# Kernel tuning notes

Hardware: AMD Instinct MI355X
Metric: run time of the kernel (lower is better)

## Reference

```python
import jax, jax.numpy as jnp
import numpy as np

D_MODEL = 1024
N_HEADS = 16
D_K = D_MODEL // N_HEADS

def _xavier(key, shape):
    fan_in, fan_out = shape[1], shape[0]
    limit = float(np.sqrt(6.0 / (fan_in + fan_out)))
    return jax.random.uniform(key, shape, jnp.float32, -limit, limit)

def setup_inputs() -> dict:
    key = jax.random.key(0)
    ks = jax.random.split(key, 7)
    B, S = 2, 2048
    return {
        "query": jax.random.normal(ks[0], (B, S, D_MODEL), jnp.float32),
        "key": jax.random.normal(ks[1], (B, S, D_MODEL), jnp.float32),
        "value": jax.random.normal(ks[2], (B, S, D_MODEL), jnp.float32),
        "w_q": _xavier(ks[3], (D_MODEL, D_MODEL)),  # torch Linear weight [out, in]
        "w_k": _xavier(ks[4], (D_MODEL, D_MODEL)),
        "w_v": _xavier(ks[5], (D_MODEL, D_MODEL)),
        "w_o": _xavier(ks[6], (D_MODEL, D_MODEL)),
        "ln_gamma": jnp.ones((D_MODEL,), jnp.float32),
        "ln_beta": jnp.zeros((D_MODEL,), jnp.float32),
    }

def reference(query, key, value, w_q, w_k, w_v, w_o, ln_gamma, ln_beta):
    B, S, _ = query.shape
    # projections (torch Linear: x @ W.T), split into heads -> [B, H, S, d_k]
    def split_heads(x, W):
        return (x @ W.T).reshape(B, S, N_HEADS, D_K).transpose(0, 2, 1, 3)
    Q = split_heads(query, w_q)
    K = split_heads(key, w_k)
    V = split_heads(value, w_v)
    scores = jnp.einsum('bhqd,bhkd->bhqk', Q, K) / jnp.sqrt(jnp.float32(D_K))
    attn = jax.nn.softmax(scores, axis=-1)  # dropout disabled (p=0 / eval)
    ctx = jnp.einsum('bhqk,bhkd->bhqd', attn, V)
    ctx = ctx.transpose(0, 2, 1, 3).reshape(B, S, D_MODEL)
    out = ctx @ w_o.T
    # residual + LayerNorm
    x = query + out
    mu = jnp.mean(x, axis=-1, keepdims=True)
    var = jnp.var(x, axis=-1, keepdims=True)
    return (x - mu) / jnp.sqrt(var + 1e-5) * ln_gamma + ln_beta
```

## Files before the change

### kernel.cpp

```cpp
#include <hip/hip_runtime.h>
#include <hip/hip_bf16.h>

#define DEVI __device__ __forceinline__

typedef float f32x4 __attribute__((ext_vector_type(4)));
typedef short bf16x8 __attribute__((ext_vector_type(8)));
typedef unsigned short ushort_t;

DEVI ushort_t f2bf(float x) {
  union { float f; unsigned u; } c; c.f = x;
  unsigned u = c.u;
  unsigned r = (u + 0x7fffu + ((u >> 16) & 1u)) >> 16;
  return (ushort_t)r;
}

DEVI float bf2f(unsigned hw) {
  union { unsigned u; float f; } c; c.u = hw << 16; return c.f;
}

DEVI unsigned cvt_pk_bf16(float lo, float hi) {
  unsigned r;
  asm volatile("v_cvt_pk_bf16_f32 %0, %1, %2" : "=v"(r) : "v"(lo), "v"(hi));
  return r;
}

DEVI void gload16(const ushort_t* g, ushort_t* l) {
  __builtin_amdgcn_global_load_lds(
      (const __attribute__((address_space(1))) unsigned int*)g,
      (__attribute__((address_space(3))) unsigned int*)l, 16, 0, 0);
}

#define WAITL0() asm volatile("s_waitcnt lgkmcnt(0)" ::: "memory")


__global__ __launch_bounds__(256)
void cvt_all_kernel(const float* __restrict__ p0, const float* __restrict__ p1,
                    const float* __restrict__ p2,
                    const float* __restrict__ w0, const float* __restrict__ w1,
                    const float* __restrict__ w2, const float* __restrict__ w3,
                    ushort_t* __restrict__ o0, ushort_t* __restrict__ o1,
                    ushort_t* __restrict__ o2,
                    ushort_t* __restrict__ q0, ushort_t* __restrict__ q1,
                    ushort_t* __restrict__ q2, ushort_t* __restrict__ q3) {
  int z = blockIdx.y;
  int i = blockIdx.x * 256 + threadIdx.x;
  const float* in;
  ushort_t* out;
  if (z < 3) {
    in = (z == 0) ? p0 : (z == 1) ? p1 : p2;
    out = (z == 0) ? o0 : (z == 1) ? o1 : o2;
  } else {
    int w = i >> 17;
    int local = i & 131071;
    in = ((w == 0) ? w0 : (w == 1) ? w1 : (w == 2) ? w2 : w3);
    out = ((w == 0) ? q0 : (w == 1) ? q1 : (w == 2) ? q2 : q3);
    i = local;
  }
  const float4* p = (const float4*)in + (size_t)i * 2;
  float4 a = p[0], b = p[1];
  uint4 v;
  v.x = cvt_pk_bf16(a.x, a.y);
  v.y = cvt_pk_bf16(a.z, a.w);
  v.z = cvt_pk_bf16(b.x, b.y);
  v.w = cvt_pk_bf16(b.z, b.w);
  ((uint4*)out)[i] = v;
}


__global__ __launch_bounds__(256)
void gemm128(const ushort_t* __restrict__ A0, const ushort_t* __restrict__ A1,
             const ushort_t* __restrict__ A2,
             const ushort_t* __restrict__ W0, const ushort_t* __restrict__ W1,
             const ushort_t* __restrict__ W2,
             void* __restrict__ O0, void* __restrict__ O1,
             void* __restrict__ O2, int mode_base, int nsteps, float qscale) {
  constexpr int K = 1024;
  int z = blockIdx.z;
  int mode = (mode_base == 3) ? 3 : mode_base + z;
  const ushort_t* A = (z == 0) ? A0 : (z == 1) ? A1 : A2;
  const ushort_t* W = (z == 0) ? W0 : (z == 1) ? W1 : W2;
  void* Op = (z == 0) ? O0 : (z == 1) ? O1 : O2;
  if (mode == 3) {
    A = A0 + z * 512;
    W = W0 + z * 512;
    Op = z ? O1 : O0;
  }
  float scale = (mode == 0) ? qscale : 1.0f;
  int m0 = (mode == 2) ? blockIdx.y * 128 : blockIdx.x * 128;
  int n0 = (mode == 2) ? blockIdx.x * 128 : blockIdx.y * 128;

  __shared__ __align__(16) ushort_t Asm[128 * 64];
  __shared__ __align__(16) ushort_t Bsm[128 * 64];

  int t = threadIdx.x;
  int lane = t & 63, wave = t >> 6;
  int wm = wave >> 1, wn = wave & 1;
  int col = lane & 15, g = lane >> 4;
  int lr = lane >> 3, lc = lane & 7;
  int cswz = col & 7;

  const ushort_t* aSrc = A + (size_t)(m0 + wave * 32 + lr) * K + (lc ^ lr) * 8;
  const ushort_t* bSrc = W + (size_t)(n0 + wave * 32 + lr) * K + (lc ^ lr) * 8;

  f32x4 z4 = {0.f, 0.f, 0.f, 0.f};
  f32x4 acc[4][4];
  for (int i = 0; i < 4; i++)
    for (int j = 0; j < 4; j++) acc[i][j] = z4;

  for (int kt = 0; kt < nsteps; ++kt) {
    int koff = kt * 64;
#pragma unroll
    for (int i_ = 0; i_ < 4; i_++) {
      gload16(aSrc + koff + i_ * 8 * K, &Asm[(wave * 32 + i_ * 8) * 64]);
      gload16(bSrc + koff + i_ * 8 * K, &Bsm[(wave * 32 + i_ * 8) * 64]);
    }
    __syncthreads();
#pragma unroll
    for (int kk = 0; kk < 2; ++kk) {
      bf16x8 af[4], bfr[4];
#pragma unroll
      for (int mi = 0; mi < 4; mi++) {
        int row = wm * 64 + mi * 16 + col;
        af[mi] = *(const bf16x8*)(Asm + row * 64 + (((kk * 4 + g) ^ cswz) * 8));
      }
#pragma unroll
      for (int ni = 0; ni < 4; ni++) {
        int row = wn * 64 + ni * 16 + col;
        bfr[ni] = *(const bf16x8*)(Bsm + row * 64 + (((kk * 4 + g) ^ cswz) * 8));
      }
      __builtin_amdgcn_s_setprio(1);
#pragma unroll
      for (int mi = 0; mi < 4; mi++)
#pragma unroll
        for (int ni = 0; ni < 4; ni++)
          acc[mi][ni] = __builtin_amdgcn_mfma_f32_16x16x32_bf16(af[mi], bfr[ni],
                                                                acc[mi][ni], 0, 0, 0);
      __builtin_amdgcn_s_setprio(0);
    }
    __syncthreads();
  }

#pragma unroll
  for (int mi = 0; mi < 4; mi++)
#pragma unroll
    for (int ni = 0; ni < 4; ni++)
#pragma unroll
      for (int r = 0; r < 4; r++) {
        int m = m0 + wm * 64 + mi * 16 + g * 4 + r;
        int n = n0 + wn * 64 + ni * 16 + col;
        float v = acc[mi][ni][r] * scale;
        if (mode <= 1) {
          int b = m >> 11, s = m & 2047, h = n >> 6, d = n & 63;
          ((ushort_t*)Op)[(((size_t)(b * 16 + h) * 2048 + s) * 64) + d] = f2bf(v);
        } else if (mode == 2) {
          int h = m >> 6, d = m & 63, b = n >> 11, s = n & 2047;
          ((ushort_t*)Op)[(((size_t)(b * 16 + h) * 64 + d) * 2048) + s] = f2bf(v);
        } else {
          ((ushort_t*)Op)[(size_t)m * 1024 + n] = f2bf(v);
        }
      }
}


__global__ __launch_bounds__(256, 4)
void attn_kernel(const ushort_t* __restrict__ Qh, const ushort_t* __restrict__ Kh,
                 const ushort_t* __restrict__ Vt,
                 ushort_t* __restrict__ op0, ushort_t* __restrict__ op1,
                 float* __restrict__ lp0, float* __restrict__ lp1) {
  int qt = blockIdx.x;
  int bh = blockIdx.y;
  int sp = blockIdx.z;
  int t = threadIdx.x, lane = t & 63, wave = t >> 6;
  int col = lane & 15, g = lane >> 4;
  int lr = lane >> 3, lc = lane & 7;
  int cswz = col & 7;
  int q0 = qt * 128 + wave * 32;
  int kbase = sp * 1024;
  ushort_t* opart = sp ? op1 : op0;
  float* lpart = sp ? lp1 : lp0;

  const ushort_t* Qp = Qh + (size_t)bh * 2048 * 64;
  const ushort_t* Kp = Kh + (size_t)bh * 2048 * 64;
  const ushort_t* Vp = Vt + (size_t)bh * 64 * 2048;

  __shared__ __align__(16) ushort_t Ksm[2][64 * 64];
  __shared__ __align__(16) ushort_t Vsm[2][64 * 64];

  int slot0 = wave * 16 + lr;
  int slot1 = slot0 + 8;
  int key0 = (slot0 & 0x20) | ((slot0 & 0x0C) << 1) | ((slot0 & 0x10) >> 2) | (slot0 & 3);
  int key1 = (slot1 & 0x20) | ((slot1 & 0x0C) << 1) | ((slot1 & 0x10) >> 2) | (slot1 & 3);

  const ushort_t* kSrc0 = Kp + (size_t)key0 * 64 + (lc ^ lr) * 8;
  const ushort_t* kSrc1 = Kp + (size_t)key1 * 64 + (lc ^ lr) * 8;
  const ushort_t* vSrc = Vp + (size_t)(wave * 16 + lr) * 2048 + (lc ^ lr) * 8;

#define ATTN_STAGE(buf, k0) do { \
    gload16(kSrc0 + (size_t)(k0) * 64, &Ksm[buf][wave * 1024]);        \
    gload16(kSrc1 + (size_t)(k0) * 64, &Ksm[buf][wave * 1024 + 512]);  \
    gload16(vSrc + (k0),               &Vsm[buf][wave * 1024]);        \
    gload16(vSrc + (k0) + 16384,       &Vsm[buf][wave * 1024 + 512]);  \
  } while (0)

  bf16x8 qa0 = *(const bf16x8*)(Qp + (size_t)(q0 + col) * 64 + g * 8);
  bf16x8 qa1 = *(const bf16x8*)(Qp + (size_t)(q0 + col) * 64 + 32 + g * 8);
  bf16x8 qb0 = *(const bf16x8*)(Qp + (size_t)(q0 + 16 + col) * 64 + g * 8);
  bf16x8 qb1 = *(const bf16x8*)(Qp + (size_t)(q0 + 16 + col) * 64 + 32 + g * 8);

  f32x4 z4 = {0.f, 0.f, 0.f, 0.f};
  f32x4 oa[4], ob[4];
  for (int i = 0; i < 4; i++) { oa[i] = z4; ob[i] = z4; }
  f32x4 la = z4, lb = z4;

  ATTN_STAGE(0, kbase);
  __syncthreads();

  for (int it = 0; it < 16; ++it) {
    int cur = it & 1;
    int k0 = kbase + it * 64;
    if (it < 15) ATTN_STAGE(cur ^ 1, k0 + 64);

    const ushort_t* Ks = Ksm[cur];
    const ushort_t* Vs = Vsm[cur];

    f32x4 sa[4], sb[4];
#pragma unroll
    for (int kt = 0; kt < 4; kt++) {
      int off = (kt * 16 + col) * 64 + ((g ^ cswz) * 8);
      bf16x8 kf0 = *(const bf16x8*)(Ks + off);
      bf16x8 kf1 = *(const bf16x8*)(Ks + (off ^ 32));
      f32x4 a = z4, b = z4;
      __builtin_amdgcn_s_setprio(1);
      a = __builtin_amdgcn_mfma_f32_16x16x32_bf16(kf0, qa0, a, 0, 0, 0);
      a = __builtin_amdgcn_mfma_f32_16x16x32_bf16(kf1, qa1, a, 0, 0, 0);
      b = __builtin_amdgcn_mfma_f32_16x16x32_bf16(kf0, qb0, b, 0, 0, 0);
      b = __builtin_amdgcn_mfma_f32_16x16x32_bf16(kf1, qb1, b, 0, 0, 0);
      __builtin_amdgcn_s_setprio(0);
      sa[kt] = a; sb[kt] = b;
    }

    unsigned pka[8], pkb[8];
#pragma unroll
    for (int kt = 0; kt < 4; kt++) {
      float a0 = __builtin_amdgcn_exp2f(sa[kt][0]);
      float a1 = __builtin_amdgcn_exp2f(sa[kt][1]);
      float a2 = __builtin_amdgcn_exp2f(sa[kt][2]);
      float a3 = __builtin_amdgcn_exp2f(sa[kt][3]);
      la[0] += a0; la[1] += a1; la[2] += a2; la[3] += a3;
      pka[2 * kt]     = cvt_pk_bf16(a0, a1);
      pka[2 * kt + 1] = cvt_pk_bf16(a2, a3);
      float b0 = __builtin_amdgcn_exp2f(sb[kt][0]);
      float b1 = __builtin_amdgcn_exp2f(sb[kt][1]);
      float b2 = __builtin_amdgcn_exp2f(sb[kt][2]);
      float b3 = __builtin_amdgcn_exp2f(sb[kt][3]);
      lb[0] += b0; lb[1] += b1; lb[2] += b2; lb[3] += b3;
      pkb[2 * kt]     = cvt_pk_bf16(b0, b1);
      pkb[2 * kt + 1] = cvt_pk_bf16(b2, b3);
    }

#pragma unroll
    for (int kk = 0; kk < 2; kk++) {
      union { uint4 u; bf16x8 f; } ua, ub;
      ua.u.x = pka[4 * kk];     ua.u.y = pka[4 * kk + 1];
      ua.u.z = pka[4 * kk + 2]; ua.u.w = pka[4 * kk + 3];
      ub.u.x = pkb[4 * kk];     ub.u.y = pkb[4 * kk + 1];
      ub.u.z = pkb[4 * kk + 2]; ub.u.w = pkb[4 * kk + 3];
      __builtin_amdgcn_s_setprio(1);
#pragma unroll
      for (int dt = 0; dt < 4; dt++) {
        bf16x8 vf = *(const bf16x8*)(Vs + (dt * 16 + col) * 64 +
                                     (((kk * 4 + g) ^ cswz) * 8));
        oa[dt] = __builtin_amdgcn_mfma_f32_16x16x32_bf16(vf, ua.f, oa[dt], 0, 0, 0);
        ob[dt] = __builtin_amdgcn_mfma_f32_16x16x32_bf16(vf, ub.f, ob[dt], 0, 0, 0);
      }
      __builtin_amdgcn_s_setprio(0);
    }
    __syncthreads();
  }
#undef ATTN_STAGE

  float lva = (la[0] + la[1]) + (la[2] + la[3]);
  lva += __shfl_xor(lva, 16);
  lva += __shfl_xor(lva, 32);
  float lvb = (lb[0] + lb[1]) + (lb[2] + lb[3]);
  lvb += __shfl_xor(lvb, 16);
  lvb += __shfl_xor(lvb, 32);
  if (g == 0) {
    lpart[(size_t)bh * 2048 + q0 + col] = lva;
    lpart[(size_t)bh * 2048 + q0 + 16 + col] = lvb;
  }
  int b = bh >> 4, h = bh & 15;
#pragma unroll
  for (int dt = 0; dt < 4; dt++)
#pragma unroll
    for (int r = 0; r < 4; r++) {
      int d = dt * 16 + g * 4 + r;
      opart[((size_t)(b * 2048 + q0 + col)) * 1024 + h * 64 + d] =
          f2bf(oa[dt][r]);
      opart[((size_t)(b * 2048 + q0 + 16 + col)) * 1024 + h * 64 + d] =
          f2bf(ob[dt][r]);
    }
}


__global__ __launch_bounds__(256)
void attn_reduce(const ushort_t* __restrict__ o0, const ushort_t* __restrict__ o1,
                 const float* __restrict__ l0, const float* __restrict__ l1,
                 ushort_t* __restrict__ ctx) {
  int m = blockIdx.x;
  int t = threadIdx.x;
  int b = m >> 11, q = m & 2047;
  int h = t >> 4;
  size_t li = (size_t)(b * 16 + h) * 2048 + q;
  float inv = 1.0f / (l0[li] + l1[li]);
  uint2 a = ((const uint2*)(o0 + (size_t)m * 1024))[t];
  uint2 c = ((const uint2*)(o1 + (size_t)m * 1024))[t];
  float x0 = (bf2f(a.x & 0xffffu) + bf2f(c.x & 0xffffu)) * inv;
  float x1 = (bf2f(a.x >> 16)     + bf2f(c.x >> 16))     * inv;
  float x2 = (bf2f(a.y & 0xffffu) + bf2f(c.y & 0xffffu)) * inv;
  float x3 = (bf2f(a.y >> 16)     + bf2f(c.y >> 16))     * inv;
  uint2 o;
  o.x = cvt_pk_bf16(x0, x1);
  o.y = cvt_pk_bf16(x2, x3);
  ((uint2*)(ctx + (size_t)m * 1024))[t] = o;
}


__global__ __launch_bounds__(256)
void ln_kernel(const float* __restrict__ resid, const ushort_t* __restrict__ p0,
               const ushort_t* __restrict__ p1,
               const float* __restrict__ gamma, const float* __restrict__ beta,
               float* __restrict__ out) {
  int m = blockIdx.x;
  int t = threadIdx.x;
  int lane = t & 63, wave = t >> 6;
  float4 a = ((const float4*)(resid + (size_t)m * 1024))[t];
  uint2 v0 = ((const uint2*)(p0 + (size_t)m * 1024))[t];
  uint2 v1 = ((const uint2*)(p1 + (size_t)m * 1024))[t];
  float4 x;
  x.x = a.x + bf2f(v0.x & 0xffffu) + bf2f(v1.x & 0xffffu);
  x.y = a.y + bf2f(v0.x >> 16)     + bf2f(v1.x >> 16);
  x.z = a.z + bf2f(v0.y & 0xffffu) + bf2f(v1.y & 0xffffu);
  x.w = a.w + bf2f(v0.y >> 16)     + bf2f(v1.y >> 16);
  float sum = (x.x + x.y) + (x.z + x.w);
  float ssq = x.x * x.x + x.y * x.y + x.z * x.z + x.w * x.w;
  for (int off = 1; off < 64; off <<= 1) {
    sum += __shfl_xor(sum, off);
    ssq += __shfl_xor(ssq, off);
  }
  __shared__ float red[8];
  if (lane == 0) { red[wave] = sum; red[4 + wave] = ssq; }
  __syncthreads();
  sum = red[0] + red[1] + red[2] + red[3];
  ssq = red[4] + red[5] + red[6] + red[7];
  float mu = sum * (1.f / 1024.f);
  float var = ssq * (1.f / 1024.f) - mu * mu;
  float rstd = rsqrtf(var + 1e-5f);
  const float4* gp = (const float4*)gamma;
  const float4* bp = (const float4*)beta;
  float4 gg = gp[t], bb = bp[t];
  float4 y;
  y.x = (x.x - mu) * rstd * gg.x + bb.x;
  y.y = (x.y - mu) * rstd * gg.y + bb.y;
  y.z = (x.z - mu) * rstd * gg.z + bb.z;
  y.w = (x.w - mu) * rstd * gg.w + bb.w;
  ((float4*)(out + (size_t)m * 1024))[t] = y;
}


extern "C" void kernel_launch(void* const* d_in, const int* in_sizes, int n_in,
                              void* d_out, int out_size, void* d_ws, size_t ws_size,
                              hipStream_t stream) {
  (void)in_sizes; (void)n_in; (void)out_size; (void)ws_size;
  const float* query = (const float*)d_in[0];
  const float* keyi  = (const float*)d_in[1];
  const float* value = (const float*)d_in[2];
  const float* w_q = (const float*)d_in[3];
  const float* w_k = (const float*)d_in[4];
  const float* w_v = (const float*)d_in[5];
  const float* w_o = (const float*)d_in[6];
  const float* ln_g = (const float*)d_in[7];
  const float* ln_b = (const float*)d_in[8];

  char* ws = (char*)d_ws;
  const size_t MB = 1u << 20;
  ushort_t* Xq  = (ushort_t*)(ws + 0 * MB);
  ushort_t* Xk  = (ushort_t*)(ws + 8 * MB);
  ushort_t* Xv  = (ushort_t*)(ws + 16 * MB);
  ushort_t* op0 = (ushort_t*)(ws + 0 * MB);
  ushort_t* op1 = (ushort_t*)(ws + 8 * MB);
  float*    l0  = (float*)   (ws + 16 * MB);
  float*    l1  = (float*)   (ws + 17 * MB);
  ushort_t* proj0 = (ushort_t*)(ws + 0 * MB);
  ushort_t* proj1 = (ushort_t*)(ws + 8 * MB);
  ushort_t* Wq  = (ushort_t*)(ws + 24 * MB);
  ushort_t* Wk  = (ushort_t*)(ws + 26 * MB);
  ushort_t* Wv  = (ushort_t*)(ws + 28 * MB);
  ushort_t* Wo  = (ushort_t*)(ws + 30 * MB);
  ushort_t* Qh  = (ushort_t*)(ws + 32 * MB);
  ushort_t* Kh  = (ushort_t*)(ws + 40 * MB);
  ushort_t* Vt  = (ushort_t*)(ws + 48 * MB);
  ushort_t* ctx = (ushort_t*)(ws + 56 * MB);

  const float SCL = 0.18033688f;

  cvt_all_kernel<<<dim3(2048, 4), 256, 0, stream>>>(
      query, keyi, value, w_q, w_k, w_v, w_o,
      Xq, Xk, Xv, Wq, Wk, Wv, Wo);

  gemm128<<<dim3(32, 8, 3), 256, 0, stream>>>(Xq, Xk, Wv, Wq, Wk, Xv,
                                              Qh, Kh, Vt, 0, 16, SCL);
  attn_kernel<<<dim3(16, 32, 2), 256, 0, stream>>>(Qh, Kh, Vt,
                                                   op0, op1, l0, l1);
  attn_reduce<<<4096, 256, 0, stream>>>(op0, op1, l0, l1, ctx);
  gemm128<<<dim3(32, 8, 2), 256, 0, stream>>>(ctx, ctx, ctx, Wo, Wo, Wo,
                                              proj0, proj1, proj0, 3, 8, 1.0f);
  ln_kernel<<<4096, 256, 0, stream>>>(query, proj0, proj1, ln_g, ln_b,
                                      (float*)d_out);
}
```

Measured before the change: 127.3 us.

## Split attention keys four ways, single-buffer LDS, raise occupancy to 8 blocks

The attention kernel now splits the key range into four chunks of 512 instead of two of 1024. It drops the double-buffered K/V staging in favour of a single LDS buffer loaded at the start of each iteration, and raises launch bounds to allow 8 blocks per CU. The grid order puts batch-head on x, and the reduction kernel sums four partial outputs and denominators. The workspace is re-laid out to hold the larger partial buffers. The aim is more concurrent waves to hide latency, but it loses load/compute overlap inside each block and doubles the partial-output traffic in the reduce step.

```diff
diff --git a/kernel.cpp b/kernel.cpp
--- a/kernel.cpp
+++ b/kernel.cpp
@@ -29,8 +29,6 @@
       (const __attribute__((address_space(1))) unsigned int*)g,
       (__attribute__((address_space(3))) unsigned int*)l, 16, 0, 0);
 }
-
-#define WAITL0() asm volatile("s_waitcnt lgkmcnt(0)" ::: "memory")
 
 
 __global__ __launch_bounds__(256)
@@ -162,29 +160,28 @@
 }
 
 
-__global__ __launch_bounds__(256, 4)
+__global__ __launch_bounds__(256, 8)
 void attn_kernel(const ushort_t* __restrict__ Qh, const ushort_t* __restrict__ Kh,
                  const ushort_t* __restrict__ Vt,
-                 ushort_t* __restrict__ op0, ushort_t* __restrict__ op1,
-                 float* __restrict__ lp0, float* __restrict__ lp1) {
-  int qt = blockIdx.x;
-  int bh = blockIdx.y;
+                 ushort_t* __restrict__ opb, float* __restrict__ lb) {
+  int bh = blockIdx.x;
+  int qt = blockIdx.y;
   int sp = blockIdx.z;
   int t = threadIdx.x, lane = t & 63, wave = t >> 6;
   int col = lane & 15, g = lane >> 4;
   int lr = lane >> 3, lc = lane & 7;
   int cswz = col & 7;
   int q0 = qt * 128 + wave * 32;
-  int kbase = sp * 1024;
-  ushort_t* opart = sp ? op1 : op0;
-  float* lpart = sp ? lp1 : lp0;
+  int kbase = sp * 512;
+  ushort_t* opart = opb + (size_t)sp * 4194304;
+  float* lpart = lb + (size_t)sp * 65536;
 
   const ushort_t* Qp = Qh + (size_t)bh * 2048 * 64;
   const ushort_t* Kp = Kh + (size_t)bh * 2048 * 64;
   const ushort_t* Vp = Vt + (size_t)bh * 64 * 2048;
 
-  __shared__ __align__(16) ushort_t Ksm[2][64 * 64];
-  __shared__ __align__(16) ushort_t Vsm[2][64 * 64];
+  __shared__ __align__(16) ushort_t Ksm[64 * 64];
+  __shared__ __align__(16) ushort_t Vsm[64 * 64];
 
   int slot0 = wave * 16 + lr;
   int slot1 = slot0 + 8;
@@ -195,13 +192,6 @@
   const ushort_t* kSrc1 = Kp + (size_t)key1 * 64 + (lc ^ lr) * 8;
   const ushort_t* vSrc = Vp + (size_t)(wave * 16 + lr) * 2048 + (lc ^ lr) * 8;
 
-#define ATTN_STAGE(buf, k0) do { \
-    gload16(kSrc0 + (size_t)(k0) * 64, &Ksm[buf][wave * 1024]);        \
-    gload16(kSrc1 + (size_t)(k0) * 64, &Ksm[buf][wave * 1024 + 512]);  \
-    gload16(vSrc + (k0),               &Vsm[buf][wave * 1024]);        \
-    gload16(vSrc + (k0) + 16384,       &Vsm[buf][wave * 1024 + 512]);  \
-  } while (0)
-
   bf16x8 qa0 = *(const bf16x8*)(Qp + (size_t)(q0 + col) * 64 + g * 8);
   bf16x8 qa1 = *(const bf16x8*)(Qp + (size_t)(q0 + col) * 64 + 32 + g * 8);
   bf16x8 qb0 = *(const bf16x8*)(Qp + (size_t)(q0 + 16 + col) * 64 + g * 8);
@@ -210,25 +200,22 @@
   f32x4 z4 = {0.f, 0.f, 0.f, 0.f};
   f32x4 oa[4], ob[4];
   for (int i = 0; i < 4; i++) { oa[i] = z4; ob[i] = z4; }
-  f32x4 la = z4, lb = z4;
-
-  ATTN_STAGE(0, kbase);
-  __syncthreads();
-
-  for (int it = 0; it < 16; ++it) {
-    int cur = it & 1;
+  f32x4 la = z4, lb4 = z4;
+
+  for (int it = 0; it < 8; ++it) {
     int k0 = kbase + it * 64;
-    if (it < 15) ATTN_STAGE(cur ^ 1, k0 + 64);
-
-    const ushort_t* Ks = Ksm[cur];
-    const ushort_t* Vs = Vsm[cur];
+    gload16(kSrc0 + (size_t)k0 * 64, &Ksm[wave * 1024]);
+    gload16(kSrc1 + (size_t)k0 * 64, &Ksm[wave * 1024 + 512]);
+    gload16(vSrc + k0,               &Vsm[wave * 1024]);
+    gload16(vSrc + k0 + 16384,       &Vsm[wave * 1024 + 512]);
+    __syncthreads();
 
     f32x4 sa[4], sb[4];
 #pragma unroll
     for (int kt = 0; kt < 4; kt++) {
       int off = (kt * 16 + col) * 64 + ((g ^ cswz) * 8);
-      bf16x8 kf0 = *(const bf16x8*)(Ks + off);
-      bf16x8 kf1 = *(const bf16x8*)(Ks + (off ^ 32));
+      bf16x8 kf0 = *(const bf16x8*)(Ksm + off);
+      bf16x8 kf1 = *(const bf16x8*)(Ksm + (off ^ 32));
       f32x4 a = z4, b = z4;
       __builtin_amdgcn_s_setprio(1);
       a = __builtin_amdgcn_mfma_f32_16x16x32_bf16(kf0, qa0, a, 0, 0, 0);
@@ -253,7 +240,7 @@
       float b1 = __builtin_amdgcn_exp2f(sb[kt][1]);
       float b2 = __builtin_amdgcn_exp2f(sb[kt][2]);
       float b3 = __builtin_amdgcn_exp2f(sb[kt][3]);
-      lb[0] += b0; lb[1] += b1; lb[2] += b2; lb[3] += b3;
+      lb4[0] += b0; lb4[1] += b1; lb4[2] += b2; lb4[3] += b3;
       pkb[2 * kt]     = cvt_pk_bf16(b0, b1);
       pkb[2 * kt + 1] = cvt_pk_bf16(b2, b3);
     }
@@ -268,7 +255,7 @@
       __builtin_amdgcn_s_setprio(1);
 #pragma unroll
       for (int dt = 0; dt < 4; dt++) {
-        bf16x8 vf = *(const bf16x8*)(Vs + (dt * 16 + col) * 64 +
+        bf16x8 vf = *(const bf16x8*)(Vsm + (dt * 16 + col) * 64 +
                                      (((kk * 4 + g) ^ cswz) * 8));
         oa[dt] = __builtin_amdgcn_mfma_f32_16x16x32_bf16(vf, ua.f, oa[dt], 0, 0, 0);
         ob[dt] = __builtin_amdgcn_mfma_f32_16x16x32_bf16(vf, ub.f, ob[dt], 0, 0, 0);
@@ -277,12 +264,11 @@
     }
     __syncthreads();
   }
-#undef ATTN_STAGE
 
   float lva = (la[0] + la[1]) + (la[2] + la[3]);
   lva += __shfl_xor(lva, 16);
   lva += __shfl_xor(lva, 32);
-  float lvb = (lb[0] + lb[1]) + (lb[2] + lb[3]);
+  float lvb = (lb4[0] + lb4[1]) + (lb4[2] + lb4[3]);
   lvb += __shfl_xor(lvb, 16);
   lvb += __shfl_xor(lvb, 32);
   if (g == 0) {
@@ -304,25 +290,32 @@
 
 
 __global__ __launch_bounds__(256)
-void attn_reduce(const ushort_t* __restrict__ o0, const ushort_t* __restrict__ o1,
-                 const float* __restrict__ l0, const float* __restrict__ l1,
+void attn_reduce(const ushort_t* __restrict__ opb, const float* __restrict__ lb,
                  ushort_t* __restrict__ ctx) {
   int m = blockIdx.x;
   int t = threadIdx.x;
   int b = m >> 11, q = m & 2047;
   int h = t >> 4;
   size_t li = (size_t)(b * 16 + h) * 2048 + q;
-  float inv = 1.0f / (l0[li] + l1[li]);
-  uint2 a = ((const uint2*)(o0 + (size_t)m * 1024))[t];
-  uint2 c = ((const uint2*)(o1 + (size_t)m * 1024))[t];
-  float x0 = (bf2f(a.x & 0xffffu) + bf2f(c.x & 0xffffu)) * inv;
-  float x1 = (bf2f(a.x >> 16)     + bf2f(c.x >> 16))     * inv;
-  float x2 = (bf2f(a.y & 0xffffu) + bf2f(c.y & 0xffffu)) * inv;
-  float x3 = (bf2f(a.y >> 16)     + bf2f(c.y >> 16))     * inv;
+  float l = lb[li] + lb[li + 65536] + lb[li + 2 * 65536] + lb[li + 3 * 65536];
+  float inv = 1.0f / l;
+  size_t idx = (size_t)m * 256 + t;
+  uint2 a0 = ((const uint2*)opb)[idx];
+  uint2 a1 = ((const uint2*)opb)[idx + 1048576];
+  uint2 a2 = ((const uint2*)opb)[idx + 2 * 1048576];
+  uint2 a3 = ((const uint2*)opb)[idx + 3 * 1048576];
+  float x0 = (bf2f(a0.x & 0xffffu) + bf2f(a1.x & 0xffffu) +
+              bf2f(a2.x & 0xffffu) + bf2f(a3.x & 0xffffu)) * inv;
+  float x1 = (bf2f(a0.x >> 16) + bf2f(a1.x >> 16) +
+              bf2f(a2.x >> 16) + bf2f(a3.x >> 16)) * inv;
+  float x2 = (bf2f(a0.y & 0xffffu) + bf2f(a1.y & 0xffffu) +
+              bf2f(a2.y & 0xffffu) + bf2f(a3.y & 0xffffu)) * inv;
+  float x3 = (bf2f(a0.y >> 16) + bf2f(a1.y >> 16) +
+              bf2f(a2.y >> 16) + bf2f(a3.y >> 16)) * inv;
   uint2 o;
   o.x = cvt_pk_bf16(x0, x1);
   o.y = cvt_pk_bf16(x2, x3);
-  ((uint2*)(ctx + (size_t)m * 1024))[t] = o;
+  ((uint2*)ctx)[idx] = o;
 }
 
 
@@ -387,20 +380,18 @@
   ushort_t* Xq  = (ushort_t*)(ws + 0 * MB);
   ushort_t* Xk  = (ushort_t*)(ws + 8 * MB);
   ushort_t* Xv  = (ushort_t*)(ws + 16 * MB);
-  ushort_t* op0 = (ushort_t*)(ws + 0 * MB);
-  ushort_t* op1 = (ushort_t*)(ws + 8 * MB);
-  float*    l0  = (float*)   (ws + 16 * MB);
-  float*    l1  = (float*)   (ws + 17 * MB);
-  ushort_t* proj0 = (ushort_t*)(ws + 0 * MB);
-  ushort_t* proj1 = (ushort_t*)(ws + 8 * MB);
-  ushort_t* Wq  = (ushort_t*)(ws + 24 * MB);
-  ushort_t* Wk  = (ushort_t*)(ws + 26 * MB);
-  ushort_t* Wv  = (ushort_t*)(ws + 28 * MB);
-  ushort_t* Wo  = (ushort_t*)(ws + 30 * MB);
+  ushort_t* opb = (ushort_t*)(ws + 0 * MB);
+  float*    lb  = (float*)   (ws + 58 * MB);
+  ushort_t* ctx = (ushort_t*)(ws + 0 * MB);
+  ushort_t* proj0 = (ushort_t*)(ws + 8 * MB);
+  ushort_t* proj1 = (ushort_t*)(ws + 16 * MB);
   ushort_t* Qh  = (ushort_t*)(ws + 32 * MB);
   ushort_t* Kh  = (ushort_t*)(ws + 40 * MB);
   ushort_t* Vt  = (ushort_t*)(ws + 48 * MB);
-  ushort_t* ctx = (ushort_t*)(ws + 56 * MB);
+  ushort_t* Wo  = (ushort_t*)(ws + 56 * MB);
+  ushort_t* Wq  = (ushort_t*)(ws + 58 * MB);
+  ushort_t* Wk  = (ushort_t*)(ws + 60 * MB);
+  ushort_t* Wv  = (ushort_t*)(ws + 62 * MB);
 
   const float SCL = 0.18033688f;
 
@@ -410,9 +401,8 @@
 
   gemm128<<<dim3(32, 8, 3), 256, 0, stream>>>(Xq, Xk, Wv, Wq, Wk, Xv,
                                               Qh, Kh, Vt, 0, 16, SCL);
-  attn_kernel<<<dim3(16, 32, 2), 256, 0, stream>>>(Qh, Kh, Vt,
-                                                   op0, op1, l0, l1);
-  attn_reduce<<<4096, 256, 0, stream>>>(op0, op1, l0, l1, ctx);
+  attn_kernel<<<dim3(32, 16, 4), 256, 0, stream>>>(Qh, Kh, Vt, opb, lb);
+  attn_reduce<<<4096, 256, 0, stream>>>(opb, lb, ctx);
   gemm128<<<dim3(32, 8, 2), 256, 0, stream>>>(ctx, ctx, ctx, Wo, Wo, Wo,
                                               proj0, proj1, proj0, 3, 8, 1.0f);
   ln_kernel<<<4096, 256, 0, stream>>>(query, proj0, proj1, ln_g, ln_b,
```

Measured after the change: 361.8 us. 184% more time.
